# Performance work log

Hardware: AMD Instinct MI355X
Metric: run time of the kernel (lower is better)

## Reference

```python
import jax, jax.numpy as jnp
import numpy as np

N = 50000      # input_dim == output_dim
E = 800000     # nnz in sparse weight (original: 12300 from w_ind.mat)
B = 64         # batch


def setup_inputs() -> dict:
    key = jax.random.key(0)
    k1, k2, k3, k4, k5 = jax.random.split(key, 5)
    inputs = jax.random.normal(k1, (B, N), dtype=jnp.float32)
    # truncated-normal(std=0.01) approximated by scaled normal
    W3 = 0.01 * jax.random.normal(k2, (E,), dtype=jnp.float32)
    b = jnp.zeros((N,), dtype=jnp.float32)
    # velocity = 1250 * row of CSV -> positive scale vector
    velocity = 1250.0 * jax.random.uniform(k3, (N,), dtype=jnp.float32)
    I = jax.random.randint(k4, (E,), 0, N, dtype=jnp.int64)  # row (dest) index
    J = jax.random.randint(k5, (E,), 0, N, dtype=jnp.int64)  # col (source) index
    return {"inputs": inputs, "W3": W3, "b": b, "velocity": velocity, "I": I, "J": J}


def reference(inputs, W3, b, velocity, I, J):
    # sparse W[i,j] = W3[e] scaled by velocity broadcast along rows -> * velocity[J]
    wv = W3 * velocity[J]                       # [E]
    # out = (W_sparse @ inputs^T)^T + b  == scatter-add over rows I
    contrib = inputs[:, J] * wv[None, :]        # [B, E] gather + scale
    out = jnp.zeros((inputs.shape[0], velocity.shape[0]), inputs.dtype)
    out = out.at[:, I].add(contrib)             # [B, N] scatter-add
    return out + b
```

## Files before the change

kernel.cpp:

```cpp
#include <hip/hip_runtime.h>


#define BATCH 64
#define SEG_ROWS 4
#define ROWS_PC 256
#define SEGS_PC 64
#define PCHUNK 2048

typedef unsigned long long ull;

__global__ void k_prep(const float* __restrict__ in, float* __restrict__ in_T,
                       int* __restrict__ coarse_hist, int NC, int N) {
    const int gid = blockIdx.x * 256 + threadIdx.x;
    if (gid < NC) coarse_hist[gid] = 0;

    __shared__ float tile[64 * 65];
    const int n0 = blockIdx.x * 64;
    const int t  = threadIdx.x;
    const int x  = t & 63;
    const int r  = t >> 6;
    for (int b = r; b < BATCH; b += 4) {
        float v = 0.f;
        if (n0 + x < N) v = in[(size_t)b * N + n0 + x];
        tile[x * 65 + b] = v;
    }
    __syncthreads();
    for (int xr = r; xr < 64; xr += 4) {
        if (n0 + xr < N) in_T[(size_t)(n0 + xr) * BATCH + x] = tile[xr * 65 + x];
    }
}

__global__ void k_hist(const int* __restrict__ I, int* __restrict__ coarse_hist, int E) {
    __shared__ int h[256];
    const int t = threadIdx.x;
    h[t] = 0;
    __syncthreads();
    const int e0 = blockIdx.x * PCHUNK;
    int e1 = e0 + PCHUNK; if (e1 > E) e1 = E;
    for (int e = e0 + t; e < e1; e += 256) atomicAdd(&h[I[e] >> 8], 1);
    __syncthreads();
    if (h[t]) atomicAdd(&coarse_hist[t], h[t]);
}

__global__ void k_scan(const int* __restrict__ coarse_hist, int* __restrict__ coarse_base,
                       int* __restrict__ gcursor, int NC) {
    __shared__ int sh[256];
    const int t = threadIdx.x;
    const int v = (t < NC) ? coarse_hist[t] : 0;
    sh[t] = v;
    __syncthreads();
    for (int off = 1; off < 256; off <<= 1) {
        const int u = (t >= off) ? sh[t - off] : 0;
        __syncthreads();
        sh[t] += u;
        __syncthreads();
    }
    if (t < NC) { coarse_base[t] = sh[t] - v; gcursor[t] = sh[t] - v; }
    if (t == NC - 1) coarse_base[NC] = sh[t];
}

__global__ void k_partition(const int* __restrict__ I, const int* __restrict__ J,
                            const float* __restrict__ W3, const float* __restrict__ velocity,
                            int* __restrict__ gcursor, ull* __restrict__ part, int E) {
    __shared__ int hist[256];
    __shared__ int base[256];
    const int t = threadIdx.x;
    hist[t] = 0;
    __syncthreads();
    const int e0 = blockIdx.x * PCHUNK;
    int e1 = e0 + PCHUNK; if (e1 > E) e1 = E;
    for (int e = e0 + t; e < e1; e += 256) atomicAdd(&hist[I[e] >> 8], 1);
    __syncthreads();
    const int cnt = hist[t];
    base[t] = cnt ? atomicAdd(&gcursor[t], cnt) : 0;
    __syncthreads();
    hist[t] = 0;
    __syncthreads();
    for (int e = e0 + t; e < e1; e += 256) {
        const int   i = I[e];
        const int   j = J[e];
        const float w = W3[e] * velocity[j];
        const int   c = i >> 8;
        const int   r = atomicAdd(&hist[c], 1);
        const unsigned lo = ((unsigned)(i & 255) << 16) | (unsigned)j;
        part[(size_t)base[c] + r] = ((ull)__float_as_uint(w) << 32) | lo;
    }
}

__global__ void k_finesort(const ull* __restrict__ part, const int* __restrict__ coarse_base,
                           ull* __restrict__ edges, int* __restrict__ seg_start) {
    const int c   = blockIdx.x;
    const int beg = coarse_base[c];
    const int end = coarse_base[c + 1];
    __shared__ int h[SEGS_PC];
    __shared__ int cur[SEGS_PC];
    const int t = threadIdx.x;
    if (t < SEGS_PC) h[t] = 0;
    __syncthreads();
    for (int e = beg + t; e < end; e += blockDim.x) {
        const unsigned lo = (unsigned)part[e];
        atomicAdd(&h[(lo >> 18) & 63], 1);
    }
    __syncthreads();
    if (t < SEGS_PC) {
        const int v = h[t];
        int s = v;
        for (int off = 1; off < SEGS_PC; off <<= 1) {
            const int u = __shfl_up(s, off);
            if (t >= off) s += u;
        }
        const int excl = s - v;
        cur[t] = excl;
        seg_start[c * SEGS_PC + t] = beg + excl;
    }
    __syncthreads();
    for (int e = beg + t; e < end; e += blockDim.x) {
        const ull rec = part[e];
        const unsigned lo = (unsigned)rec;
        const int s = (lo >> 18) & 63;
        const int pos = beg + atomicAdd(&cur[s], 1);
        edges[pos] = (rec & 0xffffffff00000000ull) | (ull)(lo & 0x3ffffu);
    }
}

__global__ void __launch_bounds__(256) k_gather(
        const float* __restrict__ in_T, const ull* __restrict__ edges,
        const int* __restrict__ seg_start, const float* __restrict__ bias,
        float* __restrict__ out, int nseg, int N) {
    __shared__ float tile[16 * 65];
    const int t    = threadIdx.x;
    const int lane = t & 63;
    const int w    = t >> 6;
    const int seg  = blockIdx.x * 4 + w;

    for (int idx = t; idx < 16 * 65; idx += 256) tile[idx] = 0.f;
    __syncthreads();

    if (seg < nseg) {
        const int wrow0 = w * 4;
        const int ebeg = seg_start[seg];
        const int eend = seg_start[seg + 1];

        for (int base = ebeg; base < eend; base += 64) {
            int cc = eend - base; if (cc > 64) cc = 64;
            ull rec = 0ull;
            if (lane < cc) rec = edges[base + lane];
            const int rlo = (int)(unsigned)(rec & 0xffffffffu);
            const int rhi = (int)(unsigned)(rec >> 32);
            for (int k0 = 0; k0 < cc; k0 += 8) {
                float v[8], ww[8]; int li[8];
                #pragma unroll
                for (int u = 0; u < 8; ++u) {
                    const int k = k0 + u;
                    const unsigned ij = (unsigned)__shfl(rlo, k);
                    ww[u] = __uint_as_float((unsigned)__shfl(rhi, k));
                    li[u] = (int)(ij >> 16);
                    const int j = (int)(ij & 0xffffu);
                    v[u] = in_T[j * BATCH + lane];
                }
                #pragma unroll
                for (int u = 0; u < 8; ++u) {
                    tile[(wrow0 + li[u]) * 65 + lane] += v[u] * ww[u];
                }
            }
        }
    }
    __syncthreads();

    const int n0  = blockIdx.x * 16;
    const int c16 = t & 15;
    const int bq  = t >> 4;
    const int n = n0 + c16;
    if (n < N) {
        const float bv = bias[n];
        for (int b = bq; b < BATCH; b += 16)
            out[(size_t)b * N + n] = tile[c16 * 65 + b] + bv;
    }
}

__global__ void k_edge_scatter_direct(const float* __restrict__ in,
                                      const float* __restrict__ W3,
                                      const float* __restrict__ velocity,
                                      const int* __restrict__ I,
                                      const int* __restrict__ J,
                                      float* __restrict__ out, int N, int E) {
    const int lane = threadIdx.x & 63;
    const long wave   = (long)blockIdx.x * (blockDim.x >> 6) + (threadIdx.x >> 6);
    const long nwaves = (long)gridDim.x * (blockDim.x >> 6);
    for (long base = wave * 64; base < E; base += nwaves * 64) {
        const long e = base + lane;
        int iv = 0, jv = 0; float wvv = 0.f;
        if (e < E) { iv = I[e]; jv = J[e]; wvv = W3[e] * velocity[jv]; }
        const int cnt = (int)((E - base) < 64 ? (E - base) : 64);
        for (int k = 0; k < cnt; ++k) {
            const int   ii = __shfl(iv, k);
            const int   jj = __shfl(jv, k);
            const float wvx = __shfl(wvv, k);
            const float val = in[(size_t)lane * N + jj] * wvx;
            atomicAdd(&out[(size_t)lane * N + ii], val);
        }
    }
}

__global__ void k_add_bias(const float* __restrict__ bias, float* __restrict__ out, int N, int total) {
    int idx = blockIdx.x * blockDim.x + threadIdx.x;
    if (idx < total) out[idx] += bias[idx % N];
}

extern "C" void kernel_launch(void* const* d_in, const int* in_sizes, int n_in,
                              void* d_out, int out_size, void* d_ws, size_t ws_size,
                              hipStream_t stream) {
    const float* inputs   = (const float*)d_in[0];
    const float* W3       = (const float*)d_in[1];
    const float* bias     = (const float*)d_in[2];
    const float* velocity = (const float*)d_in[3];
    const int*   I        = (const int*)d_in[4];
    const int*   J        = (const int*)d_in[5];
    const int E = in_sizes[1];
    const int N = in_sizes[3];
    float* out = (float*)d_out;

    const size_t mat_elems = (size_t)N * BATCH;
    const int NC   = (N + ROWS_PC - 1) / ROWS_PC;
    const int nseg = (N + SEG_ROWS - 1) / SEG_ROWS;
    const int nb_n = (N + 63) / 64;
    const int nb_e = (E + PCHUNK - 1) / PCHUNK;
    const int nb_g = (nseg + 3) / 4;

    const size_t need = mat_elems * sizeof(float)
                      + 2 * (size_t)E * sizeof(ull)
                      + (size_t)(NC + (NC + 1) + NC + NC * SEGS_PC) * sizeof(int);

    if (ws_size >= need && N <= 65535 && NC <= 256) {
        float* in_T        = (float*)d_ws;
        ull*   part        = (ull*)(in_T + mat_elems);
        ull*   edges       = part + E;
        int*   coarse_hist = (int*)(edges + E);
        int*   coarse_base = coarse_hist + NC;
        int*   gcursor     = coarse_base + NC + 1;
        int*   seg_start   = gcursor + NC;

        k_prep     <<<nb_n, 256, 0, stream>>>(inputs, in_T, coarse_hist, NC, N);
        k_hist     <<<nb_e, 256, 0, stream>>>(I, coarse_hist, E);
        k_scan     <<<1,    256, 0, stream>>>(coarse_hist, coarse_base, gcursor, NC);
        k_partition<<<nb_e, 256, 0, stream>>>(I, J, W3, velocity, gcursor, part, E);
        k_finesort <<<NC,   512, 0, stream>>>(part, coarse_base, edges, seg_start);
        k_gather   <<<nb_g, 256, 0, stream>>>(in_T, edges, seg_start, bias, out, nseg, N);
    } else {
        hipMemsetAsync(out, 0, (size_t)out_size * sizeof(float), stream);
        const int waves_needed   = (E + 63) / 64;
        const int scatter_blocks = (waves_needed + 3) / 4;
        k_edge_scatter_direct<<<scatter_blocks, 256, 0, stream>>>(inputs, W3, velocity, I, J, out, N, E);
        k_add_bias<<<(out_size + 255) / 256, 256, 0, stream>>>(bias, out, N, out_size);
    }
}
```

Before: 159.0 us.

## Drop fine sort; gather from coarse partition with LDS atomics per quarter-bucket

Removes the k_finesort pass and its second E-sized edge buffer. Each coarse bucket of 256 rows is now handled by 4 blocks of 512 threads, and each block filters for its 64-row quarter with a ballot and accumulates into shared memory with atomics. k_partition is also changed to read each edge once, keeping records in registers between the histogram and the scatter, which drops the second read pass. The cost is that every gather block reads the whole coarse bucket (4x edge reads), and shared-memory atomics replace plain adds.

```diff
diff --git a/kernel.cpp b/kernel.cpp
--- a/kernel.cpp
+++ b/kernel.cpp
@@ -2,9 +2,8 @@
 
 
 #define BATCH 64
-#define SEG_ROWS 4
 #define ROWS_PC 256
-#define SEGS_PC 64
+#define QROWS 64
 #define PCHUNK 2048
 
 typedef unsigned long long ull;
@@ -59,9 +58,10 @@
     if (t == NC - 1) coarse_base[NC] = sh[t];
 }
 
-__global__ void k_partition(const int* __restrict__ I, const int* __restrict__ J,
-                            const float* __restrict__ W3, const float* __restrict__ velocity,
-                            int* __restrict__ gcursor, ull* __restrict__ part, int E) {
+__global__ void __launch_bounds__(256) k_partition(
+        const int* __restrict__ I, const int* __restrict__ J,
+        const float* __restrict__ W3, const float* __restrict__ velocity,
+        int* __restrict__ gcursor, ull* __restrict__ part, int E) {
     __shared__ int hist[256];
     __shared__ int base[256];
     const int t = threadIdx.x;
@@ -69,112 +69,93 @@
     __syncthreads();
     const int e0 = blockIdx.x * PCHUNK;
     int e1 = e0 + PCHUNK; if (e1 > E) e1 = E;
-    for (int e = e0 + t; e < e1; e += 256) atomicAdd(&hist[I[e] >> 8], 1);
+
+    ull  rec[8];
+    int  cb[8];
+    int  rk[8];
+    bool ok[8];
+    #pragma unroll
+    for (int u = 0; u < 8; ++u) {
+        const int e = e0 + u * 256 + t;
+        ok[u] = (e < e1);
+        cb[u] = 0; rk[u] = 0; rec[u] = 0ull;
+        if (ok[u]) {
+            const int   i = I[e];
+            const int   j = J[e];
+            const float w = W3[e] * velocity[j];
+            cb[u] = i >> 8;
+            rk[u] = atomicAdd(&hist[cb[u]], 1);
+            rec[u] = ((ull)__float_as_uint(w) << 32)
+                   | ((ull)((unsigned)(i & 255) << 16) | (unsigned)j);
+        }
+    }
     __syncthreads();
     const int cnt = hist[t];
     base[t] = cnt ? atomicAdd(&gcursor[t], cnt) : 0;
     __syncthreads();
-    hist[t] = 0;
-    __syncthreads();
-    for (int e = e0 + t; e < e1; e += 256) {
-        const int   i = I[e];
-        const int   j = J[e];
-        const float w = W3[e] * velocity[j];
-        const int   c = i >> 8;
-        const int   r = atomicAdd(&hist[c], 1);
-        const unsigned lo = ((unsigned)(i & 255) << 16) | (unsigned)j;
-        part[(size_t)base[c] + r] = ((ull)__float_as_uint(w) << 32) | lo;
-    }
-}
-
-__global__ void k_finesort(const ull* __restrict__ part, const int* __restrict__ coarse_base,
-                           ull* __restrict__ edges, int* __restrict__ seg_start) {
-    const int c   = blockIdx.x;
-    const int beg = coarse_base[c];
-    const int end = coarse_base[c + 1];
-    __shared__ int h[SEGS_PC];
-    __shared__ int cur[SEGS_PC];
-    const int t = threadIdx.x;
-    if (t < SEGS_PC) h[t] = 0;
-    __syncthreads();
-    for (int e = beg + t; e < end; e += blockDim.x) {
-        const unsigned lo = (unsigned)part[e];
-        atomicAdd(&h[(lo >> 18) & 63], 1);
-    }
-    __syncthreads();
-    if (t < SEGS_PC) {
-        const int v = h[t];
-        int s = v;
-        for (int off = 1; off < SEGS_PC; off <<= 1) {
-            const int u = __shfl_up(s, off);
-            if (t >= off) s += u;
-        }
-        const int excl = s - v;
-        cur[t] = excl;
-        seg_start[c * SEGS_PC + t] = beg + excl;
-    }
-    __syncthreads();
-    for (int e = beg + t; e < end; e += blockDim.x) {
-        const ull rec = part[e];
-        const unsigned lo = (unsigned)rec;
-        const int s = (lo >> 18) & 63;
-        const int pos = beg + atomicAdd(&cur[s], 1);
-        edges[pos] = (rec & 0xffffffff00000000ull) | (ull)(lo & 0x3ffffu);
-    }
-}
-
-__global__ void __launch_bounds__(256) k_gather(
-        const float* __restrict__ in_T, const ull* __restrict__ edges,
-        const int* __restrict__ seg_start, const float* __restrict__ bias,
-        float* __restrict__ out, int nseg, int N) {
-    __shared__ float tile[16 * 65];
+    #pragma unroll
+    for (int u = 0; u < 8; ++u) {
+        if (ok[u]) part[(size_t)base[cb[u]] + rk[u]] = rec[u];
+    }
+}
+
+__global__ void __launch_bounds__(512) k_gather(
+        const float* __restrict__ in_T, const ull* __restrict__ part,
+        const int* __restrict__ coarse_base, const float* __restrict__ bias,
+        float* __restrict__ out, int N) {
+    __shared__ float tile[64 * 65];
     const int t    = threadIdx.x;
     const int lane = t & 63;
     const int w    = t >> 6;
-    const int seg  = blockIdx.x * 4 + w;
-
-    for (int idx = t; idx < 16 * 65; idx += 256) tile[idx] = 0.f;
-    __syncthreads();
-
-    if (seg < nseg) {
-        const int wrow0 = w * 4;
-        const int ebeg = seg_start[seg];
-        const int eend = seg_start[seg + 1];
-
-        for (int base = ebeg; base < eend; base += 64) {
-            int cc = eend - base; if (cc > 64) cc = 64;
-            ull rec = 0ull;
-            if (lane < cc) rec = edges[base + lane];
-            const int rlo = (int)(unsigned)(rec & 0xffffffffu);
-            const int rhi = (int)(unsigned)(rec >> 32);
-            for (int k0 = 0; k0 < cc; k0 += 8) {
-                float v[8], ww[8]; int li[8];
-                #pragma unroll
-                for (int u = 0; u < 8; ++u) {
-                    const int k = k0 + u;
-                    const unsigned ij = (unsigned)__shfl(rlo, k);
-                    ww[u] = __uint_as_float((unsigned)__shfl(rhi, k));
-                    li[u] = (int)(ij >> 16);
-                    const int j = (int)(ij & 0xffffu);
-                    v[u] = in_T[j * BATCH + lane];
+    const int c    = blockIdx.x >> 2;
+    const int q    = blockIdx.x & 3;
+
+    for (int idx = t; idx < 64 * 65; idx += 512) tile[idx] = 0.f;
+    __syncthreads();
+
+    const int beg = coarse_base[c];
+    const int end = coarse_base[c + 1];
+
+    for (int base = beg + w * 64; base < end; base += 512) {
+        int cc = end - base; if (cc > 64) cc = 64;
+        ull rec = 0ull;
+        if (lane < cc) rec = part[base + lane];
+        const int rlo = (int)(unsigned)(rec & 0xffffffffu);
+        const int rhi = (int)(unsigned)(rec >> 32);
+        const bool mine = (lane < cc) && ((((unsigned)rlo >> 22) & 3u) == (unsigned)q);
+        ull mask = __ballot(mine);
+        while (mask) {
+            float v[8], wv[8]; int li[8];
+            #pragma unroll
+            for (int u = 0; u < 8; ++u) {
+                unsigned ij = 0u, wb = 0u;
+                if (mask) {
+                    const int k = (int)__ffsll(mask) - 1;
+                    mask &= (mask - 1);
+                    ij = (unsigned)__shfl(rlo, k);
+                    wb = (unsigned)__shfl(rhi, k);
                 }
-                #pragma unroll
-                for (int u = 0; u < 8; ++u) {
-                    tile[(wrow0 + li[u]) * 65 + lane] += v[u] * ww[u];
-                }
+                wv[u] = __uint_as_float(wb);
+                li[u] = (int)((ij >> 16) & 63u);
+                const int j = (int)(ij & 0xffffu);
+                v[u] = in_T[j * BATCH + lane];
+            }
+            #pragma unroll
+            for (int u = 0; u < 8; ++u) {
+                unsafeAtomicAdd(&tile[li[u] * 65 + lane], v[u] * wv[u]);
             }
         }
     }
     __syncthreads();
 
-    const int n0  = blockIdx.x * 16;
-    const int c16 = t & 15;
-    const int bq  = t >> 4;
-    const int n = n0 + c16;
+    const int n0  = c * ROWS_PC + q * QROWS;
+    const int row = t & 63;
+    const int bq  = t >> 6;
+    const int n = n0 + row;
     if (n < N) {
         const float bv = bias[n];
-        for (int b = bq; b < BATCH; b += 16)
-            out[(size_t)b * N + n] = tile[c16 * 65 + b] + bv;
+        for (int b = bq; b < BATCH; b += 8)
+            out[(size_t)b * N + n] = tile[row * 65 + b] + bv;
     }
 }
 
@@ -222,30 +203,26 @@
 
     const size_t mat_elems = (size_t)N * BATCH;
     const int NC   = (N + ROWS_PC - 1) / ROWS_PC;
-    const int nseg = (N + SEG_ROWS - 1) / SEG_ROWS;
     const int nb_n = (N + 63) / 64;
     const int nb_e = (E + PCHUNK - 1) / PCHUNK;
-    const int nb_g = (nseg + 3) / 4;
+    const int nb_g = NC * 4;
 
     const size_t need = mat_elems * sizeof(float)
-                      + 2 * (size_t)E * sizeof(ull)
-                      + (size_t)(NC + (NC + 1) + NC + NC * SEGS_PC) * sizeof(int);
+                      + (size_t)E * sizeof(ull)
+                      + (size_t)(NC + (NC + 1) + NC) * sizeof(int);
 
     if (ws_size >= need && N <= 65535 && NC <= 256) {
         float* in_T        = (float*)d_ws;
         ull*   part        = (ull*)(in_T + mat_elems);
-        ull*   edges       = part + E;
-        int*   coarse_hist = (int*)(edges + E);
+        int*   coarse_hist = (int*)(part + E);
         int*   coarse_base = coarse_hist + NC;
         int*   gcursor     = coarse_base + NC + 1;
-        int*   seg_start   = gcursor + NC;
 
         k_prep     <<<nb_n, 256, 0, stream>>>(inputs, in_T, coarse_hist, NC, N);
         k_hist     <<<nb_e, 256, 0, stream>>>(I, coarse_hist, E);
         k_scan     <<<1,    256, 0, stream>>>(coarse_hist, coarse_base, gcursor, NC);
         k_partition<<<nb_e, 256, 0, stream>>>(I, J, W3, velocity, gcursor, part, E);
-        k_finesort <<<NC,   512, 0, stream>>>(part, coarse_base, edges, seg_start);
-        k_gather   <<<nb_g, 256, 0, stream>>>(in_T, edges, seg_start, bias, out, nseg, N);
+        k_gather   <<<nb_g, 512, 0, stream>>>(in_T, part, coarse_base, bias, out, N);
     } else {
         hipMemsetAsync(out, 0, (size_t)out_size * sizeof(float), stream);
         const int waves_needed   = (E + 63) / 64;
```

Result: slower. 548.6 us (+245.1%).
